# Performance work log

Hardware: AMD Instinct MI355X
Metric: run time of the kernel (lower is better)

Reference implementation:

```python
import jax, jax.numpy as jnp
import numpy as np
from jax import lax

POOL_SIZE = 7
MERGE_INTERVAL = 1
NUM_FRAMES = 16_777_216  # 2**24, indices exact in float32
MAX_BEATS = NUM_FRAMES // 8  # fixed upper bound on number of merged-peak sections


def setup_inputs() -> dict:
    key = jax.random.key(0)
    logit = jax.random.normal(key, (1, NUM_FRAMES), dtype=jnp.float32)
    return {"logit": logit}


def reference(logit):
    # logit: (1, N)
    x = logit[0]  # (N,)
    N = x.shape[0]
    pad = POOL_SIZE // 2
    # max_pool1d, stride 1, same padding
    pooled = lax.reduce_window(x, -jnp.inf, lax.max,
                               window_dimensions=(POOL_SIZE,),
                               window_strides=(1,),
                               padding=((pad, pad),))
    # peak: position is a local max within the window AND value > 0
    peak = (x == pooled) & (x > 0)  # (N,) bool

    idx = jnp.arange(N, dtype=jnp.int32)
    # position of the most recent peak at or before each index (-1 if none)
    last_peak = lax.cummax(jnp.where(peak, idx, jnp.int32(-1)))
    # previous peak strictly before each index
    prev_peak = jnp.concatenate([jnp.full((1,), -1, jnp.int32), last_peak[:-1]])
    gap = idx - prev_peak
    # a peak starts a new section if gap to previous peak > merge_interval (first peak always new)
    is_new = peak & ((gap > MERGE_INTERVAL) | (prev_peak < 0))
    # section id per position (valid only at peaks); sections are contiguous 0..S-1
    section = jnp.cumsum(is_new.astype(jnp.int32)) - 1
    # route non-peaks to an overflow bucket
    seg_ids = jnp.where(peak, section, jnp.int32(MAX_BEATS))

    peak_f = peak.astype(jnp.float32)
    sum_peaks = jax.ops.segment_sum(idx.astype(jnp.float32) * peak_f, seg_ids,
                                    num_segments=MAX_BEATS + 1,
                                    indices_are_sorted=True)[:MAX_BEATS]
    count_peaks = jax.ops.segment_sum(peak_f, seg_ids,
                                      num_segments=MAX_BEATS + 1,
                                      indices_are_sorted=True)[:MAX_BEATS]
    # averaged beat positions; unused sections padded with -1 (torch returns a
    # dynamically-sized (1, num_sections) tensor; here first num_sections entries match)
    beats = jnp.where(count_peaks > 0,
                      sum_peaks / jnp.maximum(count_peaks, 1.0),
                      jnp.float32(-1.0))
    return beats[None, :]  # (1, MAX_BEATS)
```

## Files before the change

### kernel.cpp

```cpp
#include <hip/hip_runtime.h>
#include <cstdint>
#include <math.h>

#define N_FRAMES 16777216
#define MAX_BEATS (N_FRAMES / 8)
#define NTHREADS 256
#define EPT 32
#define EPB (NTHREADS * EPT)
#define NBLOCKS (N_FRAMES / EPB)
#define WCHUNK 2048
#define NWCHUNK (N_FRAMES / WCHUNK)
#define NMASK32 (N_FRAMES / 32)

typedef unsigned int u32;

__global__ __launch_bounds__(NTHREADS) void k_count(const float* __restrict__ x,
                                                    int* __restrict__ counts,
                                                    u32* __restrict__ masks) {
  const int t = threadIdx.x;
  const int lane = t & 63;
  const int wv = t >> 6;
  const int q = blockIdx.x * 4 + wv;
  const int gbase = q * WCHUNK + lane * EPT;

  float v[40];
  const float4* p = reinterpret_cast<const float4*>(x + gbase);
#pragma unroll
  for (int k = 0; k < 8; ++k) {
    const float4 f = p[k];
    v[4 + 4 * k] = f.x; v[5 + 4 * k] = f.y; v[6 + 4 * k] = f.z; v[7 + 4 * k] = f.w;
  }
#pragma unroll
  for (int j = 0; j < 4; ++j) v[j] = __shfl_up(v[32 + j], 1, 64);
#pragma unroll
  for (int j = 0; j < 4; ++j) v[36 + j] = __shfl_down(v[4 + j], 1, 64);
  if (lane == 0) {
    if (gbase >= 4) {
      const float4 f = *reinterpret_cast<const float4*>(x + gbase - 4);
      v[0] = f.x; v[1] = f.y; v[2] = f.z; v[3] = f.w;
    } else {
      v[0] = v[1] = v[2] = v[3] = -INFINITY;
    }
  }
  if (lane == 63) {
    if (gbase + 36 <= N_FRAMES) {
      const float4 f = *reinterpret_cast<const float4*>(x + gbase + 32);
      v[36] = f.x; v[37] = f.y; v[38] = f.z; v[39] = f.w;
    } else {
      v[36] = v[37] = v[38] = v[39] = -INFINITY;
    }
  }

  float Lt[37];
#pragma unroll
  for (int i = 0; i < 37; ++i) Lt[i] = fmaxf(fmaxf(v[i], v[i + 1]), v[i + 2]);

  u32 pm = 0;
#pragma unroll
  for (int e = 0; e < 32; ++e) {
    const float c = v[e + 4];
    const float m = fmaxf(Lt[e + 1], Lt[e + 5]);
    if (c > 0.0f && c >= m) pm |= (1u << e);
  }
  masks[q * 64 + lane] = pm;

  u32 prevbit = __shfl_up(pm, 1, 64) >> 31;
  if (lane == 0) {
    const float c = v[3];
    const float m = fmaxf(Lt[0], Lt[4]);
    prevbit = (c > 0.0f && c >= m) ? 1u : 0u;
  }
  const u32 sm = pm & ~((pm << 1) | prevbit);
  int cnt = __popc(sm);
#pragma unroll
  for (int off = 32; off; off >>= 1) cnt += __shfl_down(cnt, off, 64);
  if (lane == 0) counts[q] = cnt;
}

__global__ __launch_bounds__(NTHREADS) void k_emit(const u32* __restrict__ masks,
                                                   const int* __restrict__ counts,
                                                   float* __restrict__ out) {
  __shared__ int s_wtot[4];
  __shared__ int s_excl0[NTHREADS];
  __shared__ int s_off[4];
  __shared__ int s_total;
  const int t = threadIdx.x;
  const int lane = t & 63;
  const int wv = t >> 6;

  int s = 0;
#pragma unroll
  for (int e = 0; e < 32; ++e) s += counts[t * 32 + e];
  int incl = s;
#pragma unroll
  for (int off = 1; off < 64; off <<= 1) {
    const int vv = __shfl_up(incl, off, 64);
    if (lane >= off) incl += vv;
  }
  s_excl0[t] = incl - s;
  if (lane == 63) s_wtot[wv] = incl;
  __syncthreads();
  if (t == 0) s_total = s_wtot[0] + s_wtot[1] + s_wtot[2] + s_wtot[3];
  const int base = blockIdx.x * 4;
  if (t < 4) {
    const int target = base + t;
    const int j = target >> 5, r = target & 31;
    int wb = 0;
    for (int ww = 0; ww < (j >> 6); ++ww) wb += s_wtot[ww];
    int pfx = wb + s_excl0[j];
    for (int e = 0; e < r; ++e) pfx += counts[j * 32 + e];
    s_off[t] = pfx;
  }
  __syncthreads();

  const int q = base + wv;
  const u32 m = masks[q * 64 + lane];
  u32 prevbit = __shfl_up(m, 1, 64) >> 31;
  if (lane == 0) prevbit = (q == 0) ? 0u : (masks[q * 64 - 1] >> 31);
  u32 sm = m & ~((m << 1) | prevbit);
  const int cnt = __popc(sm);

  int incl2 = cnt;
#pragma unroll
  for (int off = 1; off < 64; off <<= 1) {
    const int vv = __shfl_up(incl2, off, 64);
    if (lane >= off) incl2 += vv;
  }
  int sid = s_off[wv] + incl2 - cnt;

  const int gbase = q * WCHUNK + lane * 32;
  while (sm) {
    const int sb = __builtin_ctz(sm);
    sm &= sm - 1;
    const int i0 = gbase + sb;
    const u32 above = m >> sb;
    const int len = (~above == 0u) ? (32 - sb) : __builtin_ctz(~above);
    int end = i0 + len - 1;
    if (sb + len == 32) {
      int idx = q * 64 + lane + 1;
      while (idx < NMASK32) {
        const u32 mm = masks[idx];
        if (~mm == 0u) { end += 32; ++idx; }
        else { end += __builtin_ctz(~mm); break; }
      }
    }
    if (sid < MAX_BEATS)
      out[sid] = (float)(((double)i0 + (double)end) * 0.5);
    ++sid;
  }

  const int lo = blockIdx.x * (MAX_BEATS / NBLOCKS);
  const int hi = lo + (MAX_BEATS / NBLOCKS);
  for (int i = max(lo, s_total) + t; i < hi; i += NTHREADS)
    out[i] = -1.0f;
}

extern "C" void kernel_launch(void* const* d_in, const int* in_sizes, int n_in,
                              void* d_out, int out_size, void* d_ws, size_t ws_size,
                              hipStream_t stream) {
  const float* x = (const float*)d_in[0];
  float* out = (float*)d_out;

  u32* masks = (u32*)d_ws;
  int* counts = (int*)(masks + NMASK32);

  k_count<<<NBLOCKS, NTHREADS, 0, stream>>>(x, counts, masks);
  k_emit<<<NBLOCKS, NTHREADS, 0, stream>>>(masks, counts, out);
}
```

Measured before the change: 32.78 us.

## Use coalesced strided loads and ballot-based peak masks in count kernel

The count kernel now loads the input with lane-interleaved float4 accesses, so each wave reads contiguous 1 KB segments instead of each lane reading its own 128-byte chunk. Peak bits are built with wave ballots per float4 component and stored as 64-bit masks in a component-major layout. Section starts are counted from those ballots, which removes the per-lane shuffle reduction. The emit kernel rebuilds per-lane 32-bit masks with bit spreading, and walks runs that cross a lane boundary bit by bit through the new layout, which costs more for long runs.

```diff
diff --git a/kernel.cpp b/kernel.cpp
--- a/kernel.cpp
+++ b/kernel.cpp
@@ -5,118 +5,143 @@
 #define N_FRAMES 16777216
 #define MAX_BEATS (N_FRAMES / 8)
 #define NTHREADS 256
-#define EPT 32
-#define EPB (NTHREADS * EPT)
-#define NBLOCKS (N_FRAMES / EPB)
-#define WCHUNK 2048
-#define NWCHUNK (N_FRAMES / WCHUNK)
-#define NMASK32 (N_FRAMES / 32)
+#define WTILE 2048
+#define NTILE (N_FRAMES / WTILE)
+#define NBLK (NTILE / 4)
 
 typedef unsigned int u32;
+typedef unsigned long long u64;
+
+__device__ __forceinline__ float max3f(float a, float b, float c) {
+  return fmaxf(fmaxf(a, b), c);
+}
+
+__device__ __forceinline__ u32 spread4(u32 x) {
+  x = (x | (x << 12)) & 0x000F000Fu;
+  x = (x | (x << 6))  & 0x03030303u;
+  x = (x | (x << 3))  & 0x11111111u;
+  return x;
+}
+
+__device__ __forceinline__ int peak_from_masks(const u64* __restrict__ masks, int e) {
+  const int q = e >> 11, k = (e >> 8) & 7, b = e & 3, i = (e >> 2) & 63;
+  return (int)((masks[(size_t)q * 32 + k * 4 + b] >> i) & 1ull);
+}
 
 __global__ __launch_bounds__(NTHREADS) void k_count(const float* __restrict__ x,
                                                     int* __restrict__ counts,
-                                                    u32* __restrict__ masks) {
-  const int t = threadIdx.x;
-  const int lane = t & 63;
-  const int wv = t >> 6;
+                                                    u64* __restrict__ masks) {
+  const int t = threadIdx.x, lane = t & 63, wv = t >> 6;
   const int q = blockIdx.x * 4 + wv;
-  const int gbase = q * WCHUNK + lane * EPT;
+  const int base = q * WTILE;
 
-  float v[40];
-  const float4* p = reinterpret_cast<const float4*>(x + gbase);
+  float4 g[8];
+  const float4* px = reinterpret_cast<const float4*>(x + base);
+#pragma unroll
+  for (int k = 0; k < 8; ++k) g[k] = px[k * 64 + lane];
+
+  float4 eL = make_float4(-INFINITY, -INFINITY, -INFINITY, -INFINITY);
+  float4 eR = eL;
+  if (lane == 0 && base >= 4) eL = *reinterpret_cast<const float4*>(x + base - 4);
+  if (lane == 63 && base + WTILE + 4 <= N_FRAMES)
+    eR = *reinterpret_cast<const float4*>(x + base + WTILE);
+
+  bool pkm1 = false;
+  if (lane == 0) {
+    const float c = eL.w;
+    const float m = max3f(max3f(eL.x, eL.y, eL.z), g[0].x, fmaxf(g[0].y, g[0].z));
+    pkm1 = (c > 0.0f) && (c >= m);
+  }
+  u64 carry = __ballot(pkm1) & 1ull;
+
+  int cnt = 0;
 #pragma unroll
   for (int k = 0; k < 8; ++k) {
-    const float4 f = p[k];
-    v[4 + 4 * k] = f.x; v[5 + 4 * k] = f.y; v[6 + 4 * k] = f.z; v[7 + 4 * k] = f.w;
-  }
-#pragma unroll
-  for (int j = 0; j < 4; ++j) v[j] = __shfl_up(v[32 + j], 1, 64);
-#pragma unroll
-  for (int j = 0; j < 4; ++j) v[36 + j] = __shfl_down(v[4 + j], 1, 64);
-  if (lane == 0) {
-    if (gbase >= 4) {
-      const float4 f = *reinterpret_cast<const float4*>(x + gbase - 4);
-      v[0] = f.x; v[1] = f.y; v[2] = f.z; v[3] = f.w;
-    } else {
-      v[0] = v[1] = v[2] = v[3] = -INFINITY;
+    const float4 f = g[k];
+    float l1 = __shfl_up(f.y, 1, 64), l2 = __shfl_up(f.z, 1, 64), l3 = __shfl_up(f.w, 1, 64);
+    float r1 = __shfl_down(f.x, 1, 64), r2 = __shfl_down(f.y, 1, 64), r3 = __shfl_down(f.z, 1, 64);
+    float a1, a2, a3, b1, b2, b3;
+    if (k > 0) { a1 = __shfl(g[k - 1].y, 63, 64); a2 = __shfl(g[k - 1].z, 63, 64); a3 = __shfl(g[k - 1].w, 63, 64); }
+    else       { a1 = eL.y; a2 = eL.z; a3 = eL.w; }
+    if (k < 7) { b1 = __shfl(g[k + 1].x, 0, 64); b2 = __shfl(g[k + 1].y, 0, 64); b3 = __shfl(g[k + 1].z, 0, 64); }
+    else       { b1 = eR.x; b2 = eR.y; b3 = eR.z; }
+    if (lane == 0)  { l1 = a1; l2 = a2; l3 = a3; }
+    if (lane == 63) { r1 = b1; r2 = b2; r3 = b3; }
+
+    const float T0 = max3f(l1, l2, l3);
+    const float T1 = max3f(l2, l3, f.x);
+    const float T2 = max3f(l3, f.x, f.y);
+    const float T3 = max3f(f.x, f.y, f.z);
+    const float T4 = max3f(f.y, f.z, f.w);
+    const float T5 = max3f(f.z, f.w, r1);
+    const float T6 = max3f(f.w, r1, r2);
+    const float T7 = max3f(r1, r2, r3);
+    const bool p0 = (f.x > 0.0f) && (f.x >= fmaxf(T0, T4));
+    const bool p1 = (f.y > 0.0f) && (f.y >= fmaxf(T1, T5));
+    const bool p2 = (f.z > 0.0f) && (f.z >= fmaxf(T2, T6));
+    const bool p3 = (f.w > 0.0f) && (f.w >= fmaxf(T3, T7));
+    const u64 B0 = __ballot(p0), B1 = __ballot(p1), B2 = __ballot(p2), B3 = __ballot(p3);
+
+    const u64 S0 = B0 & ~((B3 << 1) | carry);
+    const u64 S1 = B1 & ~B0;
+    const u64 S2 = B2 & ~B1;
+    const u64 S3 = B3 & ~B2;
+    cnt += __popcll(S0) + __popcll(S1) + __popcll(S2) + __popcll(S3);
+    carry = B3 >> 63;
+
+    if (lane < 4) {
+      const u64 val = (lane == 0) ? B0 : (lane == 1) ? B1 : (lane == 2) ? B2 : B3;
+      masks[(size_t)q * 32 + k * 4 + lane] = val;
     }
   }
-  if (lane == 63) {
-    if (gbase + 36 <= N_FRAMES) {
-      const float4 f = *reinterpret_cast<const float4*>(x + gbase + 32);
-      v[36] = f.x; v[37] = f.y; v[38] = f.z; v[39] = f.w;
-    } else {
-      v[36] = v[37] = v[38] = v[39] = -INFINITY;
-    }
-  }
-
-  float Lt[37];
-#pragma unroll
-  for (int i = 0; i < 37; ++i) Lt[i] = fmaxf(fmaxf(v[i], v[i + 1]), v[i + 2]);
-
-  u32 pm = 0;
-#pragma unroll
-  for (int e = 0; e < 32; ++e) {
-    const float c = v[e + 4];
-    const float m = fmaxf(Lt[e + 1], Lt[e + 5]);
-    if (c > 0.0f && c >= m) pm |= (1u << e);
-  }
-  masks[q * 64 + lane] = pm;
-
-  u32 prevbit = __shfl_up(pm, 1, 64) >> 31;
-  if (lane == 0) {
-    const float c = v[3];
-    const float m = fmaxf(Lt[0], Lt[4]);
-    prevbit = (c > 0.0f && c >= m) ? 1u : 0u;
-  }
-  const u32 sm = pm & ~((pm << 1) | prevbit);
-  int cnt = __popc(sm);
-#pragma unroll
-  for (int off = 32; off; off >>= 1) cnt += __shfl_down(cnt, off, 64);
   if (lane == 0) counts[q] = cnt;
 }
 
-__global__ __launch_bounds__(NTHREADS) void k_emit(const u32* __restrict__ masks,
+__global__ __launch_bounds__(NTHREADS) void k_emit(const u64* __restrict__ masks,
                                                    const int* __restrict__ counts,
                                                    float* __restrict__ out) {
   __shared__ int s_wtot[4];
-  __shared__ int s_excl0[NTHREADS];
+  __shared__ int s_texcl[NTHREADS];
   __shared__ int s_off[4];
   __shared__ int s_total;
-  const int t = threadIdx.x;
-  const int lane = t & 63;
-  const int wv = t >> 6;
+  const int t = threadIdx.x, lane = t & 63, wv = t >> 6;
 
   int s = 0;
+  const int cb = t * 32;
 #pragma unroll
-  for (int e = 0; e < 32; ++e) s += counts[t * 32 + e];
+  for (int e = 0; e < 32; ++e) s += counts[cb + e];
   int incl = s;
 #pragma unroll
   for (int off = 1; off < 64; off <<= 1) {
     const int vv = __shfl_up(incl, off, 64);
     if (lane >= off) incl += vv;
   }
-  s_excl0[t] = incl - s;
+  s_texcl[t] = incl - s;
   if (lane == 63) s_wtot[wv] = incl;
   __syncthreads();
   if (t == 0) s_total = s_wtot[0] + s_wtot[1] + s_wtot[2] + s_wtot[3];
-  const int base = blockIdx.x * 4;
   if (t < 4) {
-    const int target = base + t;
+    const int target = blockIdx.x * 4 + t;
     const int j = target >> 5, r = target & 31;
     int wb = 0;
     for (int ww = 0; ww < (j >> 6); ++ww) wb += s_wtot[ww];
-    int pfx = wb + s_excl0[j];
+    int pfx = wb + s_texcl[j];
     for (int e = 0; e < r; ++e) pfx += counts[j * 32 + e];
     s_off[t] = pfx;
   }
   __syncthreads();
 
-  const int q = base + wv;
-  const u32 m = masks[q * 64 + lane];
+  const int q = blockIdx.x * 4 + wv;
+  const int k = lane >> 3, sh = (lane & 7) * 8;
+  const u64* mb = masks + (size_t)q * 32 + k * 4;
+  const u32 c0 = (u32)(mb[0] >> sh) & 0xFFu;
+  const u32 c1 = (u32)(mb[1] >> sh) & 0xFFu;
+  const u32 c2 = (u32)(mb[2] >> sh) & 0xFFu;
+  const u32 c3 = (u32)(mb[3] >> sh) & 0xFFu;
+  const u32 m = spread4(c0) | (spread4(c1) << 1) | (spread4(c2) << 2) | (spread4(c3) << 3);
+
   u32 prevbit = __shfl_up(m, 1, 64) >> 31;
-  if (lane == 0) prevbit = (q == 0) ? 0u : (masks[q * 64 - 1] >> 31);
+  if (lane == 0) prevbit = (q == 0) ? 0u : (u32)(masks[(size_t)q * 32 - 1] >> 63);
   u32 sm = m & ~((m << 1) | prevbit);
   const int cnt = __popc(sm);
 
@@ -128,7 +153,7 @@
   }
   int sid = s_off[wv] + incl2 - cnt;
 
-  const int gbase = q * WCHUNK + lane * 32;
+  const int gbase = q * WTILE + lane * 32;
   while (sm) {
     const int sb = __builtin_ctz(sm);
     sm &= sm - 1;
@@ -137,20 +162,16 @@
     const int len = (~above == 0u) ? (32 - sb) : __builtin_ctz(~above);
     int end = i0 + len - 1;
     if (sb + len == 32) {
-      int idx = q * 64 + lane + 1;
-      while (idx < NMASK32) {
-        const u32 mm = masks[idx];
-        if (~mm == 0u) { end += 32; ++idx; }
-        else { end += __builtin_ctz(~mm); break; }
-      }
+      int e = gbase + 32;
+      while (e < N_FRAMES && peak_from_masks(masks, e)) { end = e; ++e; }
     }
     if (sid < MAX_BEATS)
       out[sid] = (float)(((double)i0 + (double)end) * 0.5);
     ++sid;
   }
 
-  const int lo = blockIdx.x * (MAX_BEATS / NBLOCKS);
-  const int hi = lo + (MAX_BEATS / NBLOCKS);
+  const int lo = blockIdx.x * (MAX_BEATS / NBLK);
+  const int hi = lo + (MAX_BEATS / NBLK);
   for (int i = max(lo, s_total) + t; i < hi; i += NTHREADS)
     out[i] = -1.0f;
 }
@@ -161,9 +182,9 @@
   const float* x = (const float*)d_in[0];
   float* out = (float*)d_out;
 
-  u32* masks = (u32*)d_ws;
-  int* counts = (int*)(masks + NMASK32);
+  u64* masks = (u64*)d_ws;
+  int* counts = (int*)(masks + (size_t)NTILE * 32);
 
-  k_count<<<NBLOCKS, NTHREADS, 0, stream>>>(x, counts, masks);
-  k_emit<<<NBLOCKS, NTHREADS, 0, stream>>>(masks, counts, out);
+  k_count<<<NBLK, NTHREADS, 0, stream>>>(x, counts, masks);
+  k_emit<<<NBLK, NTHREADS, 0, stream>>>(masks, counts, out);
 }
```

Result: slower. 36.69 us (+11.9%).
